# Kernel tuning notes

Hardware: AMD Instinct MI355X
Metric: run time of the kernel (lower is better)

Reference implementation:

```python
import jax, jax.numpy as jnp
import numpy as np

B, T, SLATE, D = 256, 16, 20, 256
N_ITEMS, N_USERS = 100000, 10000


def setup_inputs() -> dict:
    key = jax.random.key(0)
    ks = jax.random.split(key, 8)
    s = 1.0 / np.sqrt(D)  # PyTorch GRU/Linear init scale ~ U(-1/sqrt(H), 1/sqrt(H))
    return {
        "item_idxs": jax.random.randint(ks[0], (B, T, SLATE), 0, N_ITEMS),
        "user_idxs": jax.random.randint(ks[1], (B, T), 0, N_USERS),
        "responses": jnp.zeros((B, T, SLATE), jnp.float32),
        "item_table": jax.random.normal(ks[2], (N_ITEMS, D), jnp.float32) * 0.02,
        "user_table": jax.random.normal(ks[3], (N_USERS, D), jnp.float32) * 0.02,
        "W_ih": jax.random.uniform(ks[4], (3 * D, 2 * D), jnp.float32, -s, s),
        "W_hh": jax.random.uniform(ks[5], (3 * D, D), jnp.float32, -s, s),
        "b_ih": jnp.zeros((3 * D,), jnp.float32),
        "b_hh": jnp.zeros((3 * D,), jnp.float32),
        "W_out": jax.random.uniform(ks[6], (1, D), jnp.float32, -s, s),
        "b_out": jnp.zeros((1,), jnp.float32),
    }


def _gru_cell(x, h, W_ih, W_hh, b_ih, b_hh):
    # PyTorch GRUCell math. x: [N, 2D], h: [N, D]
    gi = x @ W_ih.T + b_ih  # [N, 3D]
    gh = h @ W_hh.T + b_hh  # [N, 3D]
    i_r, i_z, i_n = jnp.split(gi, 3, axis=-1)
    h_r, h_z, h_n = jnp.split(gh, 3, axis=-1)
    r = jax.nn.sigmoid(i_r + h_r)
    z = jax.nn.sigmoid(i_z + h_z)
    n = jnp.tanh(i_n + r * h_n)
    return (1.0 - z) * n + z * h


def reference(item_idxs, user_idxs, responses, item_table, user_table,
              W_ih, W_hh, b_ih, b_hh, W_out, b_out):
    # embedding lookup: item_embs [B,T,S,D], user_embs [B,T,D]
    item_embs = item_table[item_idxs]
    user_embs = user_table[user_idxs]
    N = B * T
    e = item_embs.reshape(N, SLATE, D).transpose(1, 0, 2)  # [S, N, D]
    h0 = user_embs.reshape(N, D)
    m0 = jnp.ones((N, 1), item_embs.dtype)  # 'soft' readout multiplier, 1 at step 0

    def step(carry, e_i):
        h, m = carry
        x = jnp.concatenate([e_i, e_i * m], axis=-1)  # [N, 2D]
        h = _gru_cell(x, h, W_ih, W_hh, b_ih, b_hh)
        y = h @ W_out.T + b_out  # [N, 1]
        return (h, jax.nn.sigmoid(y)), y[:, 0]

    _, ys = jax.lax.scan(step, (h0, m0), e)  # ys: [S, N]
    return ys.transpose(1, 0).reshape(B, T, SLATE)
```

## Files before the change

### kernel.cpp

```cpp
#include <hip/hip_runtime.h>
#include <math.h>

#define SLATE 20
#define DD 256
#define NSEQ 4096

typedef __attribute__((ext_vector_type(8))) short bf16x8;
typedef __attribute__((ext_vector_type(4))) float f32x4;
typedef unsigned short u16;

__device__ __forceinline__ u16 f2bf(float f) {
    unsigned u = __float_as_uint(f);
    u += 0x7fff + ((u >> 16) & 1);
    return (u16)(u >> 16);
}
__device__ __forceinline__ float bf2f(u16 h) {
    return __uint_as_float(((unsigned)h) << 16);
}
__device__ __forceinline__ float sigmoidf_(float x) { return 1.f / (1.f + expf(-x)); }

__device__ __forceinline__ void gl_lds16(const void* g, void* l) {
    __builtin_amdgcn_global_load_lds(
        (const __attribute__((address_space(1))) unsigned int*)g,
        (__attribute__((address_space(3))) unsigned int*)l, 16, 0, 0);
}

__global__ void prep_w(const float* __restrict__ W_ih, const float* __restrict__ W_hh,
                       u16* __restrict__ W12, u16* __restrict__ Whh) {
    int i = blockIdx.x * 256 + threadIdx.x;
    if (i < 1536 * 256) {
        int j = i >> 8, k = i & 255;
        float v = (j < 768) ? W_ih[(size_t)j * 512 + k]
                            : W_ih[(size_t)(j - 768) * 512 + 256 + k];
        W12[i] = f2bf(v);
    } else {
        int i2 = i - 1536 * 256;
        Whh[i2] = f2bf(W_hh[i2]);
    }
}

__global__ void init_hm(const int* __restrict__ user_idxs, const float* __restrict__ user_table,
                        u16* __restrict__ h_bf, float* __restrict__ m) {
    int n = blockIdx.x, d = threadIdx.x;
    h_bf[(size_t)n * DD + d] = f2bf(user_table[(size_t)user_idxs[n] * DD + d]);
    if (d == 0) m[n] = 1.f;
}

__global__ void gather_e(int s0, const int* __restrict__ idxs, const float* __restrict__ itab,
                         u16* __restrict__ e_bf) {
    int g = blockIdx.x * 256 + threadIdx.x;
    int row = g >> 6, c = g & 63;
    int n = row & (NSEQ - 1), s = s0 + (row >> 12);
    int idx = idxs[n * SLATE + s];
    float4 v = *(const float4*)&itab[(size_t)idx * DD + c * 4];
    ushort4 o;
    o.x = f2bf(v.x); o.y = f2bf(v.y); o.z = f2bf(v.z); o.w = f2bf(v.w);
    *(ushort4*)&e_bf[(size_t)row * DD + c * 4] = o;
}

__global__ __launch_bounds__(256) void gemm_e(
        const u16* __restrict__ e_bf, const u16* __restrict__ W12, u16* __restrict__ Ge) {
    __shared__ u16 A_s[128][32];
    __shared__ u16 B_s[128][32];

    const int tid = threadIdx.x;
    const int w = tid >> 6, l = tid & 63, lm = l & 15, lq = l >> 4;
    const int wm = w & 1, wn = w >> 1;
    const size_t m0 = (size_t)blockIdx.y * 128;
    const size_t n0 = (size_t)blockIdx.x * 128;

    f32x4 acc[4][4];
    f32x4 zero4 = {0.f, 0.f, 0.f, 0.f};
#pragma unroll
    for (int mi = 0; mi < 4; ++mi)
#pragma unroll
        for (int nj = 0; nj < 4; ++nj) acc[mi][nj] = zero4;

    const int srow = w * 16 + (l >> 2);
    const int skc = (l & 3) * 8;
    const u16* gA = e_bf + (m0 + srow) * DD + skc;
    const u16* gB = W12 + (n0 + srow) * DD + skc;
    u16* lA = &A_s[0][0] + w * 512 + l * 8;
    u16* lB = &B_s[0][0] + w * 512 + l * 8;

    for (int kt = 0; kt < 8; ++kt) {
        const int ko = kt * 32;
        gl_lds16(gA + ko, lA);
        gl_lds16(gA + 64 * DD + ko, lA + 2048);
        gl_lds16(gB + ko, lB);
        gl_lds16(gB + 64 * DD + ko, lB + 2048);
        __syncthreads();
        bf16x8 af[4], bfr[4];
#pragma unroll
        for (int mi = 0; mi < 4; ++mi)
            af[mi] = *(const bf16x8*)&A_s[wm * 64 + mi * 16 + lm][lq * 8];
#pragma unroll
        for (int nj = 0; nj < 4; ++nj)
            bfr[nj] = *(const bf16x8*)&B_s[wn * 64 + nj * 16 + lm][lq * 8];
#pragma unroll
        for (int nj = 0; nj < 4; ++nj)
#pragma unroll
            for (int mi = 0; mi < 4; ++mi)
                acc[mi][nj] = __builtin_amdgcn_mfma_f32_16x16x32_bf16(af[mi], bfr[nj], acc[mi][nj], 0, 0, 0);
        __syncthreads();
    }

#pragma unroll
    for (int mi = 0; mi < 4; ++mi)
#pragma unroll
        for (int rr = 0; rr < 4; ++rr) {
            u16* gp = Ge + (m0 + wm * 64 + mi * 16 + lq * 4 + rr) * 1536 + n0 + wn * 64 + lm;
#pragma unroll
            for (int nj = 0; nj < 4; ++nj) gp[nj * 16] = f2bf(acc[mi][nj][rr]);
        }
}

__global__ __launch_bounds__(1024) void seq_kernel(
        int s0, int C,
        const u16* __restrict__ Ge,
        const u16* __restrict__ Whh,
        const float* __restrict__ b_ih, const float* __restrict__ b_hh,
        const float* __restrict__ W_out, const float* __restrict__ b_out,
        u16* __restrict__ h_bf, float* __restrict__ m, float* __restrict__ out)
{
    __shared__ u16   hA[8][16][32];
    __shared__ float gh_s[16][778];
    __shared__ float m_s[16];
    __shared__ float wred[16][4];

    const int tid = threadIdx.x;
    const int w = tid >> 6, l = tid & 63, lm = l & 15, lq = l >> 4;
    const int n0 = blockIdx.x * 16;
    const int jw = w * 48;
    const int d = tid & 255, sh = tid >> 8;

    {
        int r = tid >> 6, c0 = (tid & 63) * 4;
        ushort4 v = *(const ushort4*)&h_bf[(size_t)(n0 + r) * DD + c0];
        *(ushort4*)&hA[c0 >> 5][r][c0 & 31] = v;
    }
    if (tid < 16) m_s[tid] = m[n0 + tid];
    const float bi_r = b_ih[d], bi_z = b_ih[256 + d], bi_n = b_ih[512 + d];
    const float bh_r = b_hh[d], bh_z = b_hh[256 + d], bh_n = b_hh[512 + d];
    const float wo = W_out[d], bo = b_out[0];
    __syncthreads();

    for (int sc = 0; sc < C; ++sc) {
        u16 ge[4][6];
        const u16* geb = Ge + ((size_t)sc * NSEQ + n0 + sh * 4) * 1536 + d;
#pragma unroll
        for (int q = 0; q < 4; ++q)
#pragma unroll
            for (int g = 0; g < 6; ++g)
                ge[q][g] = geb[(size_t)q * 1536 + g * 256];

        f32x4 zero4 = {0.f, 0.f, 0.f, 0.f};
        f32x4 acc[3];
#pragma unroll
        for (int nj = 0; nj < 3; ++nj) acc[nj] = zero4;
#pragma unroll
        for (int kt = 0; kt < 8; ++kt) {
            bf16x8 af = *(const bf16x8*)&hA[kt][lm][lq * 8];
#pragma unroll
            for (int nj = 0; nj < 3; ++nj) {
                bf16x8 bfg = *(const bf16x8*)&Whh[(size_t)(jw + nj * 16 + lm) * DD + kt * 32 + lq * 8];
                acc[nj] = __builtin_amdgcn_mfma_f32_16x16x32_bf16(af, bfg, acc[nj], 0, 0, 0);
            }
        }
#pragma unroll
        for (int nj = 0; nj < 3; ++nj)
#pragma unroll
            for (int rr = 0; rr < 4; ++rr)
                gh_s[lq * 4 + rr][jw + nj * 16 + lm] = acc[nj][rr];
        __syncthreads();

#pragma unroll
        for (int q = 0; q < 4; ++q) {
            const int sq = sh * 4 + q;
            const float mm = m_s[sq];
            float i_r = bf2f(ge[q][0]) + mm * bf2f(ge[q][3]) + bi_r;
            float i_z = bf2f(ge[q][1]) + mm * bf2f(ge[q][4]) + bi_z;
            float i_n = bf2f(ge[q][2]) + mm * bf2f(ge[q][5]) + bi_n;
            float h_r = gh_s[sq][d] + bh_r;
            float h_z = gh_s[sq][d + 256] + bh_z;
            float h_n = gh_s[sq][d + 512] + bh_n;
            float r  = sigmoidf_(i_r + h_r);
            float z  = sigmoidf_(i_z + h_z);
            float nn = tanhf(i_n + r * h_n);
            float hold = bf2f(hA[d >> 5][sq][d & 31]);
            float hnew = (1.f - z) * nn + z * hold;
            hA[d >> 5][sq][d & 31] = f2bf(hnew);
            float yv = hnew * wo;
#pragma unroll
            for (int off = 32; off > 0; off >>= 1) yv += __shfl_down(yv, off, 64);
            if (l == 0) wred[sq][w & 3] = yv;
        }
        __syncthreads();
        if (tid < 16) {
            float y = wred[tid][0] + wred[tid][1] + wred[tid][2] + wred[tid][3] + bo;
            out[(size_t)(n0 + tid) * SLATE + (s0 + sc)] = y;
            m_s[tid] = sigmoidf_(y);
        }
        __syncthreads();
    }
    {
        int r = tid >> 6, c0 = (tid & 63) * 4;
        ushort4 v = *(const ushort4*)&hA[c0 >> 5][r][c0 & 31];
        *(ushort4*)&h_bf[(size_t)(n0 + r) * DD + c0] = v;
    }
    if (tid < 16) m[n0 + tid] = m_s[tid];
}

extern "C" void kernel_launch(void* const* d_in, const int* in_sizes, int n_in,
                              void* d_out, int out_size, void* d_ws, size_t ws_size,
                              hipStream_t stream) {
    const int*   item_idxs  = (const int*)d_in[0];
    const int*   user_idxs  = (const int*)d_in[1];
    const float* item_table = (const float*)d_in[3];
    const float* user_table = (const float*)d_in[4];
    const float* W_ih       = (const float*)d_in[5];
    const float* W_hh       = (const float*)d_in[6];
    const float* b_ih       = (const float*)d_in[7];
    const float* b_hh       = (const float*)d_in[8];
    const float* W_out      = (const float*)d_in[9];
    const float* b_out      = (const float*)d_in[10];
    float* out = (float*)d_out;

    const size_t fixed = 786432 + 393216 + 2097152 + 16384;
    static const int cands[5] = {10, 5, 4, 2, 1};
    int C = 1;
    for (int i = 0; i < 5; ++i) {
        size_t need = (size_t)cands[i] * (12582912ull + 2097152ull) + fixed;
        if (need <= ws_size) { C = cands[i]; break; }
    }

    u16*   Ge   = (u16*)d_ws;
    u16*   e_bf = (u16*)((char*)d_ws + (size_t)C * 12582912ull);
    u16*   W12  = (u16*)((char*)e_bf + (size_t)C * 2097152ull);
    u16*   Whh  = (u16*)((char*)W12 + 786432ull);
    u16*   h_bf = (u16*)((char*)Whh + 393216ull);
    float* mbuf = (float*)((char*)h_bf + 2097152ull);

    prep_w<<<2304, 256, 0, stream>>>(W_ih, W_hh, W12, Whh);
    init_hm<<<NSEQ, 256, 0, stream>>>(user_idxs, user_table, h_bf, mbuf);

    for (int s0 = 0; s0 < SLATE; s0 += C) {
        gather_e<<<C * 1024, 256, 0, stream>>>(s0, item_idxs, item_table, e_bf);
        dim3 gg(12, 32 * C);
        gemm_e<<<gg, 256, 0, stream>>>(e_bf, W12, Ge);
        seq_kernel<<<256, 1024, 0, stream>>>(s0, C, Ge, Whh, b_ih, b_hh, W_out, b_out,
                                             h_bf, mbuf, out);
    }
}
```

Before: 479.3 us.

## Remap seq_kernel so each wave owns one sequence, keep fp32 hidden state in registers

The GRU recurrence kernel is restructured so each wave handles one sequence row, with its hidden state kept in fp32 registers. The per-step output reduction becomes a single wave shuffle, which removes the wred shared array and one block barrier per step. Half of the W_hh B-fragments are preloaded into registers, biases are pre-summed into LDS, Ge is read as packed u32 pairs, and the separate init_hm launch is folded into the first seq_kernel call. The carried hidden state across chunks is now fp32 rather than bf16, which doubles that buffer and raises register pressure at 1024 threads per block.

```diff
diff --git a/kernel.cpp b/kernel.cpp
--- a/kernel.cpp
+++ b/kernel.cpp
@@ -8,6 +8,7 @@
 typedef __attribute__((ext_vector_type(8))) short bf16x8;
 typedef __attribute__((ext_vector_type(4))) float f32x4;
 typedef unsigned short u16;
+typedef unsigned int u32;
 
 __device__ __forceinline__ u16 f2bf(float f) {
     unsigned u = __float_as_uint(f);
@@ -39,13 +40,6 @@
     }
 }
 
-__global__ void init_hm(const int* __restrict__ user_idxs, const float* __restrict__ user_table,
-                        u16* __restrict__ h_bf, float* __restrict__ m) {
-    int n = blockIdx.x, d = threadIdx.x;
-    h_bf[(size_t)n * DD + d] = f2bf(user_table[(size_t)user_idxs[n] * DD + d]);
-    if (d == 0) m[n] = 1.f;
-}
-
 __global__ void gather_e(int s0, const int* __restrict__ idxs, const float* __restrict__ itab,
                          u16* __restrict__ e_bf) {
     int g = blockIdx.x * 256 + threadIdx.x;
@@ -104,7 +98,6 @@
                 acc[mi][nj] = __builtin_amdgcn_mfma_f32_16x16x32_bf16(af[mi], bfr[nj], acc[mi][nj], 0, 0, 0);
         __syncthreads();
     }
-
 #pragma unroll
     for (int mi = 0; mi < 4; ++mi)
 #pragma unroll
@@ -119,51 +112,87 @@
         int s0, int C,
         const u16* __restrict__ Ge,
         const u16* __restrict__ Whh,
+        const int* __restrict__ user_idxs, const float* __restrict__ user_table,
         const float* __restrict__ b_ih, const float* __restrict__ b_hh,
         const float* __restrict__ W_out, const float* __restrict__ b_out,
-        u16* __restrict__ h_bf, float* __restrict__ m, float* __restrict__ out)
+        float* __restrict__ h_g, float* __restrict__ m_g, float* __restrict__ out)
 {
     __shared__ u16   hA[8][16][32];
-    __shared__ float gh_s[16][778];
-    __shared__ float m_s[16];
-    __shared__ float wred[16][4];
+    __shared__ float gh_s[16][770];
+    __shared__ float bias_s[4][256];
+    __shared__ float wo_s[256];
 
     const int tid = threadIdx.x;
     const int w = tid >> 6, l = tid & 63, lm = l & 15, lq = l >> 4;
     const int n0 = blockIdx.x * 16;
-    const int jw = w * 48;
-    const int d = tid & 255, sh = tid >> 8;
-
+    const int nw = n0 + w;
+
+    if (tid < 256) bias_s[0][tid] = b_ih[tid] + b_hh[tid];
+    else if (tid < 512)  { int d = tid - 256; bias_s[1][d] = b_ih[256 + d] + b_hh[256 + d]; }
+    else if (tid < 768)  { int d = tid - 512; bias_s[2][d] = b_ih[512 + d]; }
+    else                 { int d = tid - 768; bias_s[3][d] = b_hh[512 + d]; wo_s[d] = W_out[d]; }
+
+    float h_reg[4];
+    float m_w;
     {
-        int r = tid >> 6, c0 = (tid & 63) * 4;
-        ushort4 v = *(const ushort4*)&h_bf[(size_t)(n0 + r) * DD + c0];
-        *(ushort4*)&hA[c0 >> 5][r][c0 & 31] = v;
-    }
-    if (tid < 16) m_s[tid] = m[n0 + tid];
-    const float bi_r = b_ih[d], bi_z = b_ih[256 + d], bi_n = b_ih[512 + d];
-    const float bh_r = b_hh[d], bh_z = b_hh[256 + d], bh_n = b_hh[512 + d];
-    const float wo = W_out[d], bo = b_out[0];
+        if (s0 == 0) {
+            const float* hu = user_table + (size_t)user_idxs[nw] * DD;
+            float2 a = *(const float2*)&hu[2 * l];
+            float2 b = *(const float2*)&hu[2 * l + 128];
+            h_reg[0] = a.x; h_reg[1] = a.y; h_reg[2] = b.x; h_reg[3] = b.y;
+            m_w = 1.f;
+        } else {
+            float2 a = *(const float2*)&h_g[(size_t)nw * DD + 2 * l];
+            float2 b = *(const float2*)&h_g[(size_t)nw * DD + 2 * l + 128];
+            h_reg[0] = a.x; h_reg[1] = a.y; h_reg[2] = b.x; h_reg[3] = b.y;
+            m_w = m_g[nw];
+        }
+#pragma unroll
+        for (int c = 0; c < 2; ++c) {
+            int d0 = 2 * l + 128 * c;
+            u32 pk = (u32)f2bf(h_reg[2 * c]) | ((u32)f2bf(h_reg[2 * c + 1]) << 16);
+            *(u32*)&hA[d0 >> 5][w][d0 & 31] = pk;
+        }
+    }
+
+    const u16* wbase = Whh + (size_t)(w * 48 + lm) * DD + lq * 8;
+    bf16x8 warr[12];
+#pragma unroll
+    for (int kt = 0; kt < 4; ++kt)
+#pragma unroll
+        for (int nj = 0; nj < 3; ++nj)
+            warr[kt * 3 + nj] = *(const bf16x8*)(wbase + nj * 16 * DD + kt * 32);
+
     __syncthreads();
 
+    const float bo = b_out[0];
+
     for (int sc = 0; sc < C; ++sc) {
-        u16 ge[4][6];
-        const u16* geb = Ge + ((size_t)sc * NSEQ + n0 + sh * 4) * 1536 + d;
-#pragma unroll
-        for (int q = 0; q < 4; ++q)
+        u32 ge2[2][6];
+        const u32* geb = (const u32*)(Ge + ((size_t)sc * NSEQ + nw) * 1536);
+#pragma unroll
+        for (int c = 0; c < 2; ++c)
 #pragma unroll
             for (int g = 0; g < 6; ++g)
-                ge[q][g] = geb[(size_t)q * 1536 + g * 256];
+                ge2[c][g] = geb[g * 128 + l + 64 * c];
 
         f32x4 zero4 = {0.f, 0.f, 0.f, 0.f};
         f32x4 acc[3];
 #pragma unroll
         for (int nj = 0; nj < 3; ++nj) acc[nj] = zero4;
 #pragma unroll
-        for (int kt = 0; kt < 8; ++kt) {
+        for (int kt = 0; kt < 4; ++kt) {
             bf16x8 af = *(const bf16x8*)&hA[kt][lm][lq * 8];
 #pragma unroll
+            for (int nj = 0; nj < 3; ++nj)
+                acc[nj] = __builtin_amdgcn_mfma_f32_16x16x32_bf16(af, warr[kt * 3 + nj], acc[nj], 0, 0, 0);
+        }
+#pragma unroll
+        for (int kt = 4; kt < 8; ++kt) {
+            bf16x8 af = *(const bf16x8*)&hA[kt][lm][lq * 8];
+#pragma unroll
             for (int nj = 0; nj < 3; ++nj) {
-                bf16x8 bfg = *(const bf16x8*)&Whh[(size_t)(jw + nj * 16 + lm) * DD + kt * 32 + lq * 8];
+                bf16x8 bfg = *(const bf16x8*)(wbase + nj * 16 * DD + kt * 32);
                 acc[nj] = __builtin_amdgcn_mfma_f32_16x16x32_bf16(af, bfg, acc[nj], 0, 0, 0);
             }
         }
@@ -171,44 +200,55 @@
         for (int nj = 0; nj < 3; ++nj)
 #pragma unroll
             for (int rr = 0; rr < 4; ++rr)
-                gh_s[lq * 4 + rr][jw + nj * 16 + lm] = acc[nj][rr];
-        __syncthreads();
-
-#pragma unroll
-        for (int q = 0; q < 4; ++q) {
-            const int sq = sh * 4 + q;
-            const float mm = m_s[sq];
-            float i_r = bf2f(ge[q][0]) + mm * bf2f(ge[q][3]) + bi_r;
-            float i_z = bf2f(ge[q][1]) + mm * bf2f(ge[q][4]) + bi_z;
-            float i_n = bf2f(ge[q][2]) + mm * bf2f(ge[q][5]) + bi_n;
-            float h_r = gh_s[sq][d] + bh_r;
-            float h_z = gh_s[sq][d + 256] + bh_z;
-            float h_n = gh_s[sq][d + 512] + bh_n;
-            float r  = sigmoidf_(i_r + h_r);
-            float z  = sigmoidf_(i_z + h_z);
-            float nn = tanhf(i_n + r * h_n);
-            float hold = bf2f(hA[d >> 5][sq][d & 31]);
-            float hnew = (1.f - z) * nn + z * hold;
-            hA[d >> 5][sq][d & 31] = f2bf(hnew);
-            float yv = hnew * wo;
-#pragma unroll
-            for (int off = 32; off > 0; off >>= 1) yv += __shfl_down(yv, off, 64);
-            if (l == 0) wred[sq][w & 3] = yv;
-        }
-        __syncthreads();
-        if (tid < 16) {
-            float y = wred[tid][0] + wred[tid][1] + wred[tid][2] + wred[tid][3] + bo;
-            out[(size_t)(n0 + tid) * SLATE + (s0 + sc)] = y;
-            m_s[tid] = sigmoidf_(y);
-        }
-        __syncthreads();
-    }
-    {
-        int r = tid >> 6, c0 = (tid & 63) * 4;
-        ushort4 v = *(const ushort4*)&hA[c0 >> 5][r][c0 & 31];
-        *(ushort4*)&h_bf[(size_t)(n0 + r) * DD + c0] = v;
-    }
-    if (tid < 16) m[n0 + tid] = m_s[tid];
+                gh_s[lq * 4 + rr][w * 48 + nj * 16 + lm] = acc[nj][rr];
+        __syncthreads();
+
+        float yv = 0.f;
+#pragma unroll
+        for (int c = 0; c < 2; ++c) {
+            const int d0 = 2 * l + 128 * c;
+            float g1r_lo = bf2f((u16)(ge2[c][0] & 0xffff)), g1r_hi = bf2f((u16)(ge2[c][0] >> 16));
+            float g1z_lo = bf2f((u16)(ge2[c][1] & 0xffff)), g1z_hi = bf2f((u16)(ge2[c][1] >> 16));
+            float g1n_lo = bf2f((u16)(ge2[c][2] & 0xffff)), g1n_hi = bf2f((u16)(ge2[c][2] >> 16));
+            float g2r_lo = bf2f((u16)(ge2[c][3] & 0xffff)), g2r_hi = bf2f((u16)(ge2[c][3] >> 16));
+            float g2z_lo = bf2f((u16)(ge2[c][4] & 0xffff)), g2z_hi = bf2f((u16)(ge2[c][4] >> 16));
+            float g2n_lo = bf2f((u16)(ge2[c][5] & 0xffff)), g2n_hi = bf2f((u16)(ge2[c][5] >> 16));
+            float2 hr2 = *(const float2*)&gh_s[w][d0];
+            float2 hz2 = *(const float2*)&gh_s[w][256 + d0];
+            float2 hn2 = *(const float2*)&gh_s[w][512 + d0];
+            float2 bcr = *(const float2*)&bias_s[0][d0];
+            float2 bcz = *(const float2*)&bias_s[1][d0];
+            float2 bin = *(const float2*)&bias_s[2][d0];
+            float2 bhn = *(const float2*)&bias_s[3][d0];
+            float2 wo2 = *(const float2*)&wo_s[d0];
+
+            float r_lo = sigmoidf_(g1r_lo + m_w * g2r_lo + hr2.x + bcr.x);
+            float r_hi = sigmoidf_(g1r_hi + m_w * g2r_hi + hr2.y + bcr.y);
+            float z_lo = sigmoidf_(g1z_lo + m_w * g2z_lo + hz2.x + bcz.x);
+            float z_hi = sigmoidf_(g1z_hi + m_w * g2z_hi + hz2.y + bcz.y);
+            float n_lo = tanhf(g1n_lo + m_w * g2n_lo + bin.x + r_lo * (hn2.x + bhn.x));
+            float n_hi = tanhf(g1n_hi + m_w * g2n_hi + bin.y + r_hi * (hn2.y + bhn.y));
+            float hn_lo = (1.f - z_lo) * n_lo + z_lo * h_reg[2 * c];
+            float hn_hi = (1.f - z_hi) * n_hi + z_hi * h_reg[2 * c + 1];
+            h_reg[2 * c] = hn_lo; h_reg[2 * c + 1] = hn_hi;
+            u32 pk = (u32)f2bf(hn_lo) | ((u32)f2bf(hn_hi) << 16);
+            *(u32*)&hA[d0 >> 5][w][d0 & 31] = pk;
+            yv += hn_lo * wo2.x + hn_hi * wo2.y;
+        }
+#pragma unroll
+        for (int off = 32; off > 0; off >>= 1) yv += __shfl_xor(yv, off, 64);
+        float y = yv + bo;
+        if (l == 0) out[(size_t)nw * SLATE + (s0 + sc)] = y;
+        m_w = sigmoidf_(y);
+        __syncthreads();
+    }
+
+#pragma unroll
+    for (int c = 0; c < 2; ++c) {
+        float2 v; v.x = h_reg[2 * c]; v.y = h_reg[2 * c + 1];
+        *(float2*)&h_g[(size_t)nw * DD + 2 * l + 128 * c] = v;
+    }
+    if (l == 0) m_g[nw] = m_w;
 }
 
 extern "C" void kernel_launch(void* const* d_in, const int* in_sizes, int n_in,
@@ -226,7 +266,7 @@
     const float* b_out      = (const float*)d_in[10];
     float* out = (float*)d_out;
 
-    const size_t fixed = 786432 + 393216 + 2097152 + 16384;
+    const size_t fixed = 786432ull + 393216ull + 4194304ull + 16384ull;
     static const int cands[5] = {10, 5, 4, 2, 1};
     int C = 1;
     for (int i = 0; i < 5; ++i) {
@@ -238,17 +278,16 @@
     u16*   e_bf = (u16*)((char*)d_ws + (size_t)C * 12582912ull);
     u16*   W12  = (u16*)((char*)e_bf + (size_t)C * 2097152ull);
     u16*   Whh  = (u16*)((char*)W12 + 786432ull);
-    u16*   h_bf = (u16*)((char*)Whh + 393216ull);
-    float* mbuf = (float*)((char*)h_bf + 2097152ull);
+    float* h_g  = (float*)((char*)Whh + 393216ull);
+    float* m_g  = (float*)((char*)h_g + 4194304ull);
 
     prep_w<<<2304, 256, 0, stream>>>(W_ih, W_hh, W12, Whh);
-    init_hm<<<NSEQ, 256, 0, stream>>>(user_idxs, user_table, h_bf, mbuf);
 
     for (int s0 = 0; s0 < SLATE; s0 += C) {
         gather_e<<<C * 1024, 256, 0, stream>>>(s0, item_idxs, item_table, e_bf);
         dim3 gg(12, 32 * C);
         gemm_e<<<gg, 256, 0, stream>>>(e_bf, W12, Ge);
-        seq_kernel<<<256, 1024, 0, stream>>>(s0, C, Ge, Whh, b_ih, b_hh, W_out, b_out,
-                                             h_bf, mbuf, out);
-    }
-}
+        seq_kernel<<<256, 1024, 0, stream>>>(s0, C, Ge, Whh, user_idxs, user_table,
+                                             b_ih, b_hh, W_out, b_out, h_g, m_g, out);
+    }
+}
```

Result: faster. 451.0 us (-5.9%).
